# Performance work log

Hardware: AMD Instinct MI355X
Metric: run time of the kernel (lower is better)

## Reference

```python
import jax, jax.numpy as jnp
import numpy as np

SELF_DIM = 6   # self_state_dim
HID = 50       # lstm_hidden_dim


def setup_inputs() -> dict:
    key = jax.random.key(0)
    ks = jax.random.split(key, 16)
    B, N, D = 8192, 64, 13  # batch, num humans, joint-state length

    def w(k, shape):
        # kaiming-ish init, stored as [in, out] so forward is x @ W + b
        return jax.random.normal(k, shape, jnp.float32) / jnp.sqrt(jnp.float32(shape[0]))

    z = lambda n: jnp.zeros((n,), jnp.float32)
    return {
        "state": jax.random.normal(ks[0], (B, N, D), jnp.float32),
        # mlp1: 13 -> 150 -> 100, last_relu=True
        "mlp1_w1": w(ks[1], (13, 150)),  "mlp1_b1": z(150),
        "mlp1_w2": w(ks[2], (150, 100)), "mlp1_b2": z(100),
        # attention: 200 -> 100 -> 100 -> 1 (no relu on last)
        "attn_w1": w(ks[3], (200, 100)), "attn_b1": z(100),
        "attn_w2": w(ks[4], (100, 100)), "attn_b2": z(100),
        "attn_w3": w(ks[5], (100, 1)),   "attn_b3": z(1),
        # LSTM(input=7, hidden=50), torch gate order i,f,g,o
        "lstm_wih": w(ks[6], (7, 4 * HID)),
        "lstm_whh": w(ks[7], (HID, 4 * HID)),
        "lstm_bih": z(4 * HID), "lstm_bhh": z(4 * HID),
        # mlp: 56 -> 150 -> 100 -> 100 -> 1
        "mlp_w1": w(ks[8], (SELF_DIM + HID, 150)), "mlp_b1": z(150),
        "mlp_w2": w(ks[9], (150, 100)),            "mlp_b2": z(100),
        "mlp_w3": w(ks[10], (100, 100)),           "mlp_b3": z(100),
        "mlp_w4": w(ks[11], (100, 1)),             "mlp_b4": z(1),
    }


def reference(state, mlp1_w1, mlp1_b1, mlp1_w2, mlp1_b2,
              attn_w1, attn_b1, attn_w2, attn_b2, attn_w3, attn_b3,
              lstm_wih, lstm_whh, lstm_bih, lstm_bhh,
              mlp_w1, mlp_b1, mlp_w2, mlp_b2, mlp_w3, mlp_b3, mlp_w4, mlp_b4):
    relu = jax.nn.relu
    B, N, D = state.shape
    self_state = state[:, 0, :SELF_DIM]      # [B, 6]
    human_state = state[:, :, SELF_DIM:]     # [B, N, 7]

    # mlp1 over all B*N per-human joint-state rows (last_relu=True)
    flat = state.reshape(B * N, D)
    m1 = relu(relu(flat @ mlp1_w1 + mlp1_b1) @ mlp1_w2 + mlp1_b2)   # [B*N, 100]

    # mean-pooled global state, broadcast back per human, concat, attention score
    gdim = m1.shape[-1]
    global_state = jnp.mean(m1.reshape(B, N, gdim), axis=1, keepdims=True)
    global_state = jnp.broadcast_to(global_state, (B, N, gdim)).reshape(B * N, gdim)
    a_in = jnp.concatenate([m1, global_state], axis=1)               # [B*N, 200]
    scores = (relu(relu(a_in @ attn_w1 + attn_b1) @ attn_w2 + attn_b2) @ attn_w3 + attn_b3)
    scores = scores.reshape(B, N)
    # NOTE: in the original torch code `scores` only feed `rerank_human_state`,
    # which is never consumed (dead code) -- the LSTM runs on the UNSORTED
    # human_state. We keep the score computation for fidelity; the per-sample
    # argsort/gather is dropped since it does not affect the output.

    # LSTM over the N humans (batch_first in torch, h0=c0=0)
    xs = jnp.transpose(human_state, (1, 0, 2))   # [N, B, 7]
    h0 = jnp.zeros((B, HID), state.dtype)

    def step(carry, x_t):
        h, c = carry
        gates = x_t @ lstm_wih + h @ lstm_whh + lstm_bih + lstm_bhh  # [B, 4H]
        i, f, g, o = jnp.split(gates, 4, axis=-1)
        c = jax.nn.sigmoid(f) * c + jax.nn.sigmoid(i) * jnp.tanh(g)
        h = jax.nn.sigmoid(o) * jnp.tanh(c)
        return (h, c), None

    (hn, _cn), _ = jax.lax.scan(step, (h0, h0), xs)

    # value head on [self_state, h_n]
    joint = jnp.concatenate([self_state, hn], axis=1)   # [B, 56]
    x = relu(joint @ mlp_w1 + mlp_b1)
    x = relu(x @ mlp_w2 + mlp_b2)
    x = relu(x @ mlp_w3 + mlp_b3)
    value = x @ mlp_w4 + mlp_b4                          # [B, 1]
    return value
```

## Files before the change

kernel.cpp:

```cpp
#include <hip/hip_runtime.h>

typedef __attribute__((ext_vector_type(8))) short short8;
typedef __attribute__((ext_vector_type(4))) float f32x4;
union frag_u { short8 v; unsigned short u[8]; };

__device__ __forceinline__ float bf2f(unsigned short b) {
  unsigned int u = ((unsigned int)b) << 16;
  float f; __builtin_memcpy(&f, &u, 4); return f;
}
__device__ __forceinline__ unsigned short f2bf(float f) {
  unsigned int u; __builtin_memcpy(&u, &f, 4);
  return (unsigned short)((u + 0x7FFFu + ((u >> 16) & 1u)) >> 16);
}
__device__ __forceinline__ unsigned short hi_of(float f) { return f2bf(f); }
__device__ __forceinline__ unsigned short lo_of(float f) {
  unsigned short h = f2bf(f); return f2bf(f - bf2f(h));
}
__device__ __forceinline__ float sigm(float x) {
  return __builtin_amdgcn_rcpf(1.f + __expf(-x));
}
__device__ __forceinline__ float tanh_(float x) {
  return 1.f - 2.f * __builtin_amdgcn_rcpf(1.f + __expf(2.f * x));
}

__global__ void detect_dtype_kernel(const unsigned short* s, int* flag) {
  if (threadIdx.x == 0 && blockIdx.x == 0) {
    int insane = 0;
    for (int i = 0; i < 64; ++i) {
      unsigned short v = s[2 * i];
      int e = (v >> 7) & 0xFF;
      if (e < 100 || e > 140) insane++;
    }
    *flag = (insane >= 16) ? 1 : 0;
  }
}

template <int AS, typename GetB, typename GetW>
__device__ __forceinline__ void mfma_layer(const unsigned short* sA, float* sG,
    int wave, int col, int quad, int kc_n, int ntiles, int N, GetB getb, GetW getw)
{
  for (int tile = wave; tile < ntiles; tile += 16) {
    int n = tile * 16 + col;
    float b = (n < N) ? getb(n) : 0.f;
    f32x4 acc = {b, b, b, b};
    for (int kc = 0; kc < kc_n; ++kc) {
      short8 a = *(const short8*)&sA[col * AS + kc * 32 + quad * 8];
      frag_u w;
      #pragma unroll
      for (int j = 0; j < 8; ++j) {
        int k = kc * 32 + quad * 8 + j;
        w.u[j] = (n < N) ? getw(k, n) : (unsigned short)0;
      }
      acc = __builtin_amdgcn_mfma_f32_16x16x32_bf16(a, w.v, acc, 0, 0, 0);
    }
    *(f32x4*)&sG[n * 20 + quad * 4] = acc;
  }
}

template <int AS, bool LO>
__device__ __forceinline__ void relu_fill(const float* sG, unsigned short* sA,
                                          int tid, int N, int loOff, int Kpad) {
  for (int idx = tid; idx < 16 * Kpad; idx += 1024) {
    int m = idx & 15, n = idx >> 4;
    unsigned short v = 0;
    if (n < N) {
      v = f2bf(fmaxf(sG[n * 20 + m], 0.f));
    } else if (LO && n >= loOff && n < loOff + N) {
      float x = fmaxf(sG[(n - loOff) * 20 + m], 0.f);
      v = lo_of(x);
    }
    sA[m * AS + n] = v;
  }
}

template <bool F32>
__global__ __launch_bounds__(1024, 8) void value_net_kernel(
    const void* state_, const void* wih_, const void* whh_,
    const void* bih_, const void* bhh_,
    const void* w1_, const void* b1_, const void* w2_, const void* b2_,
    const void* w3_, const void* b3_, const void* w4_, const void* b4_,
    void* out_, const int* flag)
{
  if (flag && *flag != (F32 ? 1 : 0)) return;

  constexpr int AS = F32 ? 328 : 168;
  constexpr int KC = F32 ? 6 : 4;

  __shared__ __align__(16) unsigned short sA[16 * AS];
  __shared__ __align__(16) float sG[208 * 20];

  const unsigned short* st16 = (const unsigned short*)state_;
  const float*          stf  = (const float*)state_;

  const int tid  = threadIdx.x;
  const int wave = tid >> 6;
  const int lane = tid & 63;
  const int col  = lane & 15;
  const int quad = lane >> 4;
  const int r0   = blockIdx.x * 16;

  {
    unsigned int* a32 = (unsigned int*)sA;
    constexpr int ZN = (16 * AS / 2 + 1023) / 1024;
    #pragma unroll
    for (int i = 0; i < ZN; ++i) {
      int idx = tid + i * 1024;
      if (idx < 16 * AS / 2) a32[idx] = 0;
    }
  }

  auto W_lstm = [&](int k, int n) -> unsigned short {
    if constexpr (!F32) {
      const unsigned short* wih = (const unsigned short*)wih_;
      const unsigned short* whh = (const unsigned short*)whh_;
      if (k < 7)   return wih[k * 200 + n];
      if (k < 57)  return whh[(k - 7) * 200 + n];
      if (k < 107) return whh[(k - 57) * 200 + n];
      return (unsigned short)0;
    } else {
      const float* wih = (const float*)wih_;
      const float* whh = (const float*)whh_;
      if (k < 7)   return hi_of(wih[k * 200 + n]);
      if (k < 14)  return hi_of(wih[(k - 7) * 200 + n]);
      if (k < 21)  return lo_of(wih[(k - 14) * 200 + n]);
      if (k < 71)  return hi_of(whh[(k - 21) * 200 + n]);
      if (k < 121) return hi_of(whh[(k - 71) * 200 + n]);
      if (k < 171) return lo_of(whh[(k - 121) * 200 + n]);
      return (unsigned short)0;
    }
  };
  auto ldf = [&](const void* p, int i) -> float {
    if constexpr (F32) return ((const float*)p)[i];
    else               return bf2f(((const unsigned short*)p)[i]);
  };

  const bool hasTile = (wave < 13);
  frag_u wf[KC];
  float  wb = 0.f;
  if (hasTile) {
    int n = wave * 16 + col;
    #pragma unroll
    for (int kc = 0; kc < KC; ++kc) {
      #pragma unroll
      for (int j = 0; j < 8; ++j) {
        int k = kc * 32 + quad * 8 + j;
        wf[kc].u[j] = (n < 200) ? W_lstm(k, n) : (unsigned short)0;
      }
    }
    wb = (n < 200) ? (ldf(bih_, n) + ldf(bhh_, n)) : 0.f;
  }

  const bool iv = tid < 800;
  const int  im = tid & 15, iu = tid >> 4;
  float c_ = 0.f, hf = 0.f;

  const bool isx = (tid >= 800) && (tid < 912);
  const int  xm = (tid - 800) / 7, xd = (tid - 800) - ((tid - 800) / 7) * 7;
  auto xgidx = [&](int t) -> size_t { return (size_t)(r0 + xm) * 832 + t * 13 + 6 + xd; };
  auto xwrite = [&](float fv, unsigned short bv) {
    if constexpr (!F32) { sA[xm * AS + xd] = bv; }
    else {
      unsigned short h = f2bf(fv);
      sA[xm * AS + xd] = h; sA[xm * AS + 14 + xd] = h;
      sA[xm * AS + 7 + xd] = f2bf(fv - bf2f(h));
    }
  };

  unsigned short xv16 = 0; float xvf = 0.f;

  __syncthreads();
  if (isx) {
    if constexpr (!F32) { xwrite(0.f, st16[xgidx(0)]); xv16 = st16[xgidx(1)]; }
    else                { xwrite(stf[xgidx(0)], 0);    xvf  = stf[xgidx(1)]; }
  }
  __syncthreads();

  for (int t = 0; t < 64; ++t) {
    if (hasTile) {
      short8 a[KC];
      #pragma unroll
      for (int kc = 0; kc < KC; ++kc)
        a[kc] = *(const short8*)&sA[col * AS + kc * 32 + quad * 8];
      f32x4 acc = {wb, wb, wb, wb};
      #pragma unroll
      for (int kc = 0; kc < KC; ++kc)
        acc = __builtin_amdgcn_mfma_f32_16x16x32_bf16(a[kc], wf[kc].v, acc, 0, 0, 0);
      int n = wave * 16 + col;
      *(f32x4*)&sG[n * 20 + quad * 4] = acc;
    }
    __syncthreads();
    if (iv) {
      float gi = sG[iu * 20 + im];
      float gf = sG[(50 + iu) * 20 + im];
      float gg = sG[(100 + iu) * 20 + im];
      float go = sG[(150 + iu) * 20 + im];
      float cc = sigm(gf) * c_ + sigm(gi) * tanh_(gg);
      c_ = cc;
      float h = sigm(go) * tanh_(cc);
      if (t < 63) {
        unsigned short hb = f2bf(h);
        unsigned short hl = f2bf(h - bf2f(hb));
        if constexpr (!F32) { sA[im * AS + 7 + iu] = hb; sA[im * AS + 57 + iu] = hl; }
        else { sA[im * AS + 21 + iu] = hb; sA[im * AS + 121 + iu] = hb; sA[im * AS + 71 + iu] = hl; }
      } else hf = h;
    }
    if (isx && t < 63) {
      if constexpr (!F32) xwrite(0.f, xv16); else xwrite(xvf, 0);
      if (t < 62) { if constexpr (!F32) xv16 = st16[xgidx(t + 2)]; else xvf = stf[xgidx(t + 2)]; }
    }
    __syncthreads();
  }

  {
    unsigned int* a32 = (unsigned int*)sA;
    constexpr int ZN = (16 * AS / 2 + 1023) / 1024;
    #pragma unroll
    for (int i = 0; i < ZN; ++i) {
      int idx = tid + i * 1024;
      if (idx < 16 * AS / 2) a32[idx] = 0;
    }
  }
  __syncthreads();
  if (iv) {
    unsigned short hb = f2bf(hf);
    unsigned short hl = f2bf(hf - bf2f(hb));
    sA[im * AS + 6 + iu] = hb;
    if constexpr (!F32) sA[im * AS + 56 + iu] = hl; else sA[im * AS + 62 + iu] = hl;
  }
  if (tid < 96) {
    int m = tid / 6, d = tid - (tid / 6) * 6;
    if constexpr (!F32) sA[m * AS + d] = st16[(size_t)(r0 + m) * 832 + d];
    else {
      float f = stf[(size_t)(r0 + m) * 832 + d];
      sA[m * AS + d] = hi_of(f); sA[m * AS + 56 + d] = lo_of(f);
    }
  }
  __syncthreads();

  mfma_layer<AS>(sA, sG, wave, col, quad, 4, 10, 150,
    [&](int n) { return ldf(b1_, n); },
    [&](int k, int n) -> unsigned short {
      if constexpr (!F32) {
        const unsigned short* w1 = (const unsigned short*)w1_;
        if (k < 56)  return w1[k * 150 + n];
        if (k < 106) return w1[(k - 50) * 150 + n];
        return (unsigned short)0;
      } else {
        const float* w1 = (const float*)w1_;
        if (k < 56)  return hi_of(w1[k * 150 + n]);
        if (k < 112) return hi_of(w1[(k - 56) * 150 + n]);
        return (unsigned short)0;
      }
    });
  __syncthreads();
  if constexpr (!F32) relu_fill<AS, false>(sG, sA, tid, 150, 160, 160);
  else                relu_fill<AS, true >(sG, sA, tid, 150, 150, 320);
  __syncthreads();

  mfma_layer<AS>(sA, sG, wave, col, quad, F32 ? 10 : 5, 7, 100,
    [&](int n) { return ldf(b2_, n); },
    [&](int k, int n) -> unsigned short {
      if constexpr (!F32) {
        const unsigned short* w2 = (const unsigned short*)w2_;
        return (k < 150) ? w2[k * 100 + n] : (unsigned short)0;
      } else {
        const float* w2 = (const float*)w2_;
        if (k < 150) return hi_of(w2[k * 100 + n]);
        if (k < 300) return hi_of(w2[(k - 150) * 100 + n]);
        return (unsigned short)0;
      }
    });
  __syncthreads();
  if constexpr (!F32) relu_fill<AS, false>(sG, sA, tid, 100, 128, 128);
  else                relu_fill<AS, true >(sG, sA, tid, 100, 100, 224);
  __syncthreads();

  mfma_layer<AS>(sA, sG, wave, col, quad, F32 ? 7 : 4, 7, 100,
    [&](int n) { return ldf(b3_, n); },
    [&](int k, int n) -> unsigned short {
      if constexpr (!F32) {
        const unsigned short* w3 = (const unsigned short*)w3_;
        return (k < 100) ? w3[k * 100 + n] : (unsigned short)0;
      } else {
        const float* w3 = (const float*)w3_;
        if (k < 100) return hi_of(w3[k * 100 + n]);
        if (k < 200) return hi_of(w3[(k - 100) * 100 + n]);
        return (unsigned short)0;
      }
    });
  __syncthreads();

  if (tid < 256) {
    int m = tid >> 4, j0 = tid & 15;
    float s = 0.f;
    for (int j = j0; j < 100; j += 16)
      s += fmaxf(sG[j * 20 + m], 0.f) * ldf(w4_, j);
    s += __shfl_xor(s, 8); s += __shfl_xor(s, 4);
    s += __shfl_xor(s, 2); s += __shfl_xor(s, 1);
    if (j0 == 0) {
      float v = s + ldf(b4_, 0);
      if constexpr (!F32) ((unsigned short*)out_)[r0 + m] = f2bf(v);
      else                ((float*)out_)[r0 + m] = v;
    }
  }
}

extern "C" void kernel_launch(void* const* d_in, const int* in_sizes, int n_in,
                              void* d_out, int out_size, void* d_ws, size_t ws_size,
                              hipStream_t stream) {
  (void)in_sizes; (void)n_in; (void)out_size;
  const void* state = d_in[0];
  const void* wih = d_in[11]; const void* whh = d_in[12];
  const void* bih = d_in[13]; const void* bhh = d_in[14];
  const void* w1  = d_in[15]; const void* b1  = d_in[16];
  const void* w2  = d_in[17]; const void* b2  = d_in[18];
  const void* w3  = d_in[19]; const void* b3  = d_in[20];
  const void* w4  = d_in[21]; const void* b4  = d_in[22];

  if (ws_size >= sizeof(int)) {
    int* flag = (int*)d_ws;
    detect_dtype_kernel<<<dim3(1), dim3(64), 0, stream>>>(
        (const unsigned short*)state, flag);
    value_net_kernel<false><<<dim3(512), dim3(1024), 0, stream>>>(
        state, wih, whh, bih, bhh, w1, b1, w2, b2, w3, b3, w4, b4, d_out, flag);
    value_net_kernel<true><<<dim3(512), dim3(1024), 0, stream>>>(
        state, wih, whh, bih, bhh, w1, b1, w2, b2, w3, b3, w4, b4, d_out, flag);
  } else {
    value_net_kernel<false><<<dim3(512), dim3(1024), 0, stream>>>(
        state, wih, whh, bih, bhh, w1, b1, w2, b2, w3, b3, w4, b4, d_out,
        (const int*)nullptr);
  }
}
```

Baseline: 241.2 us.

## Double-buffer LSTM state tile, fuse gate activation into MFMA waves, pick dtype on host

Permutes the LSTM weight columns so each MFMA wave's output tile holds the i/f/g/o gates of the same hidden units. The same wave can then apply the cell update right after its MFMA, with no separate activation phase. The shared input tile is double-buffered, so the loop needs one barrier per timestep instead of two. The host now picks the fp32 or bf16 kernel from the input byte size, skipping the detect kernel and the idle second launch, and the detect kernel itself now uses a wave ballot. In exchange, activations run on the 13 MFMA waves (which have 4 idle lanes among them) instead of 800 dedicated threads, and LDS use roughly doubles for the input tile.

```diff
diff --git a/kernel.cpp b/kernel.cpp
--- a/kernel.cpp
+++ b/kernel.cpp
@@ -24,15 +24,11 @@
 }
 
 __global__ void detect_dtype_kernel(const unsigned short* s, int* flag) {
-  if (threadIdx.x == 0 && blockIdx.x == 0) {
-    int insane = 0;
-    for (int i = 0; i < 64; ++i) {
-      unsigned short v = s[2 * i];
-      int e = (v >> 7) & 0xFF;
-      if (e < 100 || e > 140) insane++;
-    }
-    *flag = (insane >= 16) ? 1 : 0;
-  }
+  int i = threadIdx.x;
+  unsigned short v = s[2 * i];
+  int e = (v >> 7) & 0xFF;
+  unsigned long long m = __ballot(e < 100 || e > 140);
+  if (i == 0) *flag = (__popcll(m) >= 16) ? 1 : 0;
 }
 
 template <int AS, typename GetB, typename GetW>
@@ -86,7 +82,7 @@
   constexpr int AS = F32 ? 328 : 168;
   constexpr int KC = F32 ? 6 : 4;
 
-  __shared__ __align__(16) unsigned short sA[16 * AS];
+  __shared__ __align__(16) unsigned short sA[2][16 * AS];
   __shared__ __align__(16) float sG[208 * 20];
 
   const unsigned short* st16 = (const unsigned short*)state_;
@@ -100,12 +96,12 @@
   const int r0   = blockIdx.x * 16;
 
   {
-    unsigned int* a32 = (unsigned int*)sA;
-    constexpr int ZN = (16 * AS / 2 + 1023) / 1024;
+    unsigned int* a32 = (unsigned int*)&sA[0][0];
+    constexpr int ZT = 16 * AS;
     #pragma unroll
-    for (int i = 0; i < ZN; ++i) {
+    for (int i = 0; i < (ZT + 1023) / 1024; ++i) {
       int idx = tid + i * 1024;
-      if (idx < 16 * AS / 2) a32[idx] = 0;
+      if (idx < ZT) a32[idx] = 0;
     }
   }
 
@@ -138,106 +134,112 @@
   frag_u wf[KC];
   float  wb = 0.f;
   if (hasTile) {
-    int n = wave * 16 + col;
+    int nn = wave * 16 + col;
+    int no = (nn < 200) ? ((nn & 3) * 50 + (nn >> 2)) : 0;
     #pragma unroll
     for (int kc = 0; kc < KC; ++kc) {
       #pragma unroll
       for (int j = 0; j < 8; ++j) {
         int k = kc * 32 + quad * 8 + j;
-        wf[kc].u[j] = (n < 200) ? W_lstm(k, n) : (unsigned short)0;
-      }
-    }
-    wb = (n < 200) ? (ldf(bih_, n) + ldf(bhh_, n)) : 0.f;
-  }
-
-  const bool iv = tid < 800;
-  const int  im = tid & 15, iu = tid >> 4;
+        wf[kc].u[j] = (nn < 200) ? W_lstm(k, no) : (unsigned short)0;
+      }
+    }
+    wb = (nn < 200) ? (ldf(bih_, no) + ldf(bhh_, no)) : 0.f;
+  }
+
+  const int  u_   = wave * 4 + quad;
+  const bool iact = hasTile && (u_ < 50);
   float c_ = 0.f, hf = 0.f;
 
-  const bool isx = (tid >= 800) && (tid < 912);
-  const int  xm = (tid - 800) / 7, xd = (tid - 800) - ((tid - 800) / 7) * 7;
+  const bool isx = (tid >= 832) && (tid < 944);
+  const int  xm = (tid - 832) / 7, xd = (tid - 832) - ((tid - 832) / 7) * 7;
   auto xgidx = [&](int t) -> size_t { return (size_t)(r0 + xm) * 832 + t * 13 + 6 + xd; };
-  auto xwrite = [&](float fv, unsigned short bv) {
-    if constexpr (!F32) { sA[xm * AS + xd] = bv; }
+  auto xwrite = [&](unsigned short* sAw, float fv, unsigned short bv) {
+    if constexpr (!F32) { sAw[xm * AS + xd] = bv; }
     else {
       unsigned short h = f2bf(fv);
-      sA[xm * AS + xd] = h; sA[xm * AS + 14 + xd] = h;
-      sA[xm * AS + 7 + xd] = f2bf(fv - bf2f(h));
+      sAw[xm * AS + xd] = h; sAw[xm * AS + 14 + xd] = h;
+      sAw[xm * AS + 7 + xd] = f2bf(fv - bf2f(h));
     }
   };
-
   unsigned short xv16 = 0; float xvf = 0.f;
 
   __syncthreads();
   if (isx) {
-    if constexpr (!F32) { xwrite(0.f, st16[xgidx(0)]); xv16 = st16[xgidx(1)]; }
-    else                { xwrite(stf[xgidx(0)], 0);    xvf  = stf[xgidx(1)]; }
+    if constexpr (!F32) { xwrite(&sA[0][0], 0.f, st16[xgidx(0)]); xv16 = st16[xgidx(1)]; }
+    else                { xwrite(&sA[0][0], stf[xgidx(0)], 0);    xvf  = stf[xgidx(1)]; }
   }
   __syncthreads();
 
   for (int t = 0; t < 64; ++t) {
+    const unsigned short* sAr = &sA[t & 1][0];
+    unsigned short*       sAw = &sA[(t & 1) ^ 1][0];
+
     if (hasTile) {
       short8 a[KC];
       #pragma unroll
       for (int kc = 0; kc < KC; ++kc)
-        a[kc] = *(const short8*)&sA[col * AS + kc * 32 + quad * 8];
+        a[kc] = *(const short8*)&sAr[col * AS + kc * 32 + quad * 8];
       f32x4 acc = {wb, wb, wb, wb};
       #pragma unroll
       for (int kc = 0; kc < KC; ++kc)
         acc = __builtin_amdgcn_mfma_f32_16x16x32_bf16(a[kc], wf[kc].v, acc, 0, 0, 0);
-      int n = wave * 16 + col;
-      *(f32x4*)&sG[n * 20 + quad * 4] = acc;
+      *(f32x4*)&sG[(wave * 16 + col) * 20 + quad * 4] = acc;
+
+      if (iact) {
+        int nb = (wave * 16 + quad * 4);
+        float gi = sG[(nb + 0) * 20 + col];
+        float gf = sG[(nb + 1) * 20 + col];
+        float gg = sG[(nb + 2) * 20 + col];
+        float go = sG[(nb + 3) * 20 + col];
+        float cc = sigm(gf) * c_ + sigm(gi) * tanh_(gg);
+        c_ = cc;
+        float h = sigm(go) * tanh_(cc);
+        if (t < 63) {
+          unsigned short hb = f2bf(h);
+          unsigned short hl = f2bf(h - bf2f(hb));
+          if constexpr (!F32) {
+            sAw[col * AS + 7 + u_] = hb; sAw[col * AS + 57 + u_] = hl;
+          } else {
+            sAw[col * AS + 21 + u_] = hb; sAw[col * AS + 121 + u_] = hb;
+            sAw[col * AS + 71 + u_] = hl;
+          }
+        } else hf = h;
+      }
+    } else if (isx && t < 63) {
+      if constexpr (!F32) xwrite(sAw, 0.f, xv16); else xwrite(sAw, xvf, 0);
+      if (t < 62) { if constexpr (!F32) xv16 = st16[xgidx(t + 2)]; else xvf = stf[xgidx(t + 2)]; }
     }
     __syncthreads();
-    if (iv) {
-      float gi = sG[iu * 20 + im];
-      float gf = sG[(50 + iu) * 20 + im];
-      float gg = sG[(100 + iu) * 20 + im];
-      float go = sG[(150 + iu) * 20 + im];
-      float cc = sigm(gf) * c_ + sigm(gi) * tanh_(gg);
-      c_ = cc;
-      float h = sigm(go) * tanh_(cc);
-      if (t < 63) {
-        unsigned short hb = f2bf(h);
-        unsigned short hl = f2bf(h - bf2f(hb));
-        if constexpr (!F32) { sA[im * AS + 7 + iu] = hb; sA[im * AS + 57 + iu] = hl; }
-        else { sA[im * AS + 21 + iu] = hb; sA[im * AS + 121 + iu] = hb; sA[im * AS + 71 + iu] = hl; }
-      } else hf = h;
-    }
-    if (isx && t < 63) {
-      if constexpr (!F32) xwrite(0.f, xv16); else xwrite(xvf, 0);
-      if (t < 62) { if constexpr (!F32) xv16 = st16[xgidx(t + 2)]; else xvf = stf[xgidx(t + 2)]; }
-    }
-    __syncthreads();
-  }
-
+  }
+
+  unsigned short* sA0 = &sA[0][0];
   {
-    unsigned int* a32 = (unsigned int*)sA;
-    constexpr int ZN = (16 * AS / 2 + 1023) / 1024;
+    unsigned int* a32 = (unsigned int*)sA0;
     #pragma unroll
-    for (int i = 0; i < ZN; ++i) {
+    for (int i = 0; i < (16 * AS / 2 + 1023) / 1024; ++i) {
       int idx = tid + i * 1024;
       if (idx < 16 * AS / 2) a32[idx] = 0;
     }
   }
   __syncthreads();
-  if (iv) {
+  if (iact) {
     unsigned short hb = f2bf(hf);
     unsigned short hl = f2bf(hf - bf2f(hb));
-    sA[im * AS + 6 + iu] = hb;
-    if constexpr (!F32) sA[im * AS + 56 + iu] = hl; else sA[im * AS + 62 + iu] = hl;
+    sA0[col * AS + 6 + u_] = hb;
+    if constexpr (!F32) sA0[col * AS + 56 + u_] = hl; else sA0[col * AS + 62 + u_] = hl;
   }
   if (tid < 96) {
     int m = tid / 6, d = tid - (tid / 6) * 6;
-    if constexpr (!F32) sA[m * AS + d] = st16[(size_t)(r0 + m) * 832 + d];
+    if constexpr (!F32) sA0[m * AS + d] = st16[(size_t)(r0 + m) * 832 + d];
     else {
       float f = stf[(size_t)(r0 + m) * 832 + d];
-      sA[m * AS + d] = hi_of(f); sA[m * AS + 56 + d] = lo_of(f);
-    }
-  }
-  __syncthreads();
-
-  mfma_layer<AS>(sA, sG, wave, col, quad, 4, 10, 150,
+      sA0[m * AS + d] = hi_of(f); sA0[m * AS + 56 + d] = lo_of(f);
+    }
+  }
+  __syncthreads();
+
+  mfma_layer<AS>(sA0, sG, wave, col, quad, 4, 10, 150,
     [&](int n) { return ldf(b1_, n); },
     [&](int k, int n) -> unsigned short {
       if constexpr (!F32) {
@@ -253,11 +255,11 @@
       }
     });
   __syncthreads();
-  if constexpr (!F32) relu_fill<AS, false>(sG, sA, tid, 150, 160, 160);
-  else                relu_fill<AS, true >(sG, sA, tid, 150, 150, 320);
-  __syncthreads();
-
-  mfma_layer<AS>(sA, sG, wave, col, quad, F32 ? 10 : 5, 7, 100,
+  if constexpr (!F32) relu_fill<AS, false>(sG, sA0, tid, 150, 160, 160);
+  else                relu_fill<AS, true >(sG, sA0, tid, 150, 150, 320);
+  __syncthreads();
+
+  mfma_layer<AS>(sA0, sG, wave, col, quad, F32 ? 10 : 5, 7, 100,
     [&](int n) { return ldf(b2_, n); },
     [&](int k, int n) -> unsigned short {
       if constexpr (!F32) {
@@ -271,11 +273,11 @@
       }
     });
   __syncthreads();
-  if constexpr (!F32) relu_fill<AS, false>(sG, sA, tid, 100, 128, 128);
-  else                relu_fill<AS, true >(sG, sA, tid, 100, 100, 224);
-  __syncthreads();
-
-  mfma_layer<AS>(sA, sG, wave, col, quad, F32 ? 7 : 4, 7, 100,
+  if constexpr (!F32) relu_fill<AS, false>(sG, sA0, tid, 100, 128, 128);
+  else                relu_fill<AS, true >(sG, sA0, tid, 100, 100, 224);
+  __syncthreads();
+
+  mfma_layer<AS>(sA0, sG, wave, col, quad, F32 ? 7 : 4, 7, 100,
     [&](int n) { return ldf(b3_, n); },
     [&](int k, int n) -> unsigned short {
       if constexpr (!F32) {
@@ -308,7 +310,7 @@
 extern "C" void kernel_launch(void* const* d_in, const int* in_sizes, int n_in,
                               void* d_out, int out_size, void* d_ws, size_t ws_size,
                               hipStream_t stream) {
-  (void)in_sizes; (void)n_in; (void)out_size;
+  (void)n_in; (void)out_size;
   const void* state = d_in[0];
   const void* wih = d_in[11]; const void* whh = d_in[12];
   const void* bih = d_in[13]; const void* bhh = d_in[14];
@@ -317,7 +319,19 @@
   const void* w3  = d_in[19]; const void* b3  = d_in[20];
   const void* w4  = d_in[21]; const void* b4  = d_in[22];
 
-  if (ws_size >= sizeof(int)) {
+  const long long F32B  = 8192LL * 64 * 13 * 4;
+  const long long BF16B = 8192LL * 64 * 13 * 2;
+  long long sz = in_sizes ? (long long)in_sizes[0] : -1;
+
+  if (sz == F32B) {
+    value_net_kernel<true><<<dim3(512), dim3(1024), 0, stream>>>(
+        state, wih, whh, bih, bhh, w1, b1, w2, b2, w3, b3, w4, b4, d_out,
+        (const int*)nullptr);
+  } else if (sz == BF16B) {
+    value_net_kernel<false><<<dim3(512), dim3(1024), 0, stream>>>(
+        state, wih, whh, bih, bhh, w1, b1, w2, b2, w3, b3, w4, b4, d_out,
+        (const int*)nullptr);
+  } else if (ws_size >= sizeof(int)) {
     int* flag = (int*)d_ws;
     detect_dtype_kernel<<<dim3(1), dim3(64), 0, stream>>>(
         (const unsigned short*)state, flag);
```

Result: faster. 230.2 us (-4.6%).
